# Kernel tuning notes

Hardware: AMD Instinct MI355X
Metric: run time of the kernel (lower is better)

## Reference

```python
import math
import numpy as np
import jax
import jax.numpy as jnp

B_IN, B_OUT, B_INV = 64, 20, 20
BATCH, F_IN, F_OUT = 16, 16, 32
N_GRID = 24
SCALING = 1.0 / math.sqrt(N_GRID * F_IN * B_OUT ** 4.0 / B_IN ** 2.0)


def _make_grid():
    # s2 near-identity grid: 3 betas (up to pi/8) x 8 alphas -> (beta, alpha) pairs
    beta = np.arange(1, 4) * (np.pi / 8) / 3
    alpha = np.linspace(0, 2 * np.pi, 8, endpoint=False)
    B, A = np.meshgrid(beta, alpha, indexing='ij')
    return np.stack((B.ravel(), A.ravel()), axis=1)  # [24, 2]


def _wigner_d(l, betas):
    """Full Wigner-d matrices d^l_{m,n}(beta): [n_beta, 2l+1, 2l+1], m,n in -l..l."""
    nb = betas.shape[0]
    cb, sb = np.cos(betas / 2.0), np.sin(betas / 2.0)
    lg = [math.lgamma(k + 1) for k in range(2 * l + 1)]
    d = np.zeros((nb, 2 * l + 1, 2 * l + 1))
    for mi, m in enumerate(range(-l, l + 1)):
        for ni, n in enumerate(range(-l, l + 1)):
            pref = 0.5 * (lg[l + m] + lg[l - m] + lg[l + n] + lg[l - n])
            val = np.zeros(nb)
            for s in range(max(0, n - m), min(l + n, l - m) + 1):
                c = pref - (lg[l + n - s] + lg[s] + lg[m - n + s] + lg[l - m - s])
                val += ((-1.0) ** (m - n + s)) * np.exp(c) * cb ** (2 * l + n - m - 2 * s) * sb ** (m - n + 2 * s)
            d[:, mi, ni] = val
    return d


def _quadrature_weights(b):
    # SOFT quadrature weights over the 2b beta samples
    k = np.arange(b)
    theta = np.pi * (2 * np.arange(2 * b) + 1) / (4.0 * b)
    return np.array([(2.0 / b) * np.sin(t) * np.sum(np.sin((2 * k + 1) * t) / (2 * k + 1)) for t in theta])


def _setup_constants():
    # S2 analysis weights: quadrature-weighted d^l_{m,0}(beta_j), laid out as l-blocks (start l^2, width 2l+1)
    betas_in = np.pi * (2 * np.arange(2 * B_IN) + 1) / (4.0 * B_IN)
    w = _quadrature_weights(B_IN)
    cols = [_wigner_d(l, betas_in)[:, :, l] * w[:, None] for l in range(B_OUT)]
    w_s2 = np.concatenate(cols, axis=1)  # [2*B_IN, B_OUT**2]

    # kernel spherical-harmonic sampling matrix F[p, lm] = d^l_{m,0}(beta_p) * exp(-i m alpha_p)
    grid = _make_grid()
    blocks = []
    for l in range(B_OUT):
        dk = _wigner_d(l, grid[:, 0])[:, :, l]  # [P, 2l+1]
        m = np.arange(-l, l + 1)
        blocks.append(dk * np.exp(-1j * m[None, :] * grid[:, 1:2]))
    F_k = np.concatenate(blocks, axis=1)  # [P, B_OUT**2] complex

    # SO(3) synthesis: (2l+1) * d^l_{m,n}(beta_j) on the output beta grid
    betas_inv = np.pi * (2 * np.arange(2 * B_INV) + 1) / (4.0 * B_INV)
    d_inv = [(2 * l + 1) * _wigner_d(l, betas_inv) for l in range(B_OUT)]
    return (jnp.asarray(w_s2, jnp.float32),
            jnp.asarray(F_k, jnp.complex64),
            [jnp.asarray(d, jnp.float32) for d in d_inv])


_CONSTS = None


def _consts():
    global _CONSTS
    if _CONSTS is None:
        _CONSTS = _setup_constants()
    return _CONSTS


def _forward(x, kernel, bias, w_s2, F_k, d_inv):
    # S2 FFT over alpha: x [batch, f_in, 2b_in(beta), 2b_in(alpha)] -> complex freq bins
    xf = jnp.fft.fft(x.astype(jnp.complex64), axis=-1)
    # kernel spectrum y^l_m: [nspec, f_in, f_out]
    y = jnp.einsum('iop,pm->mio', (kernel * SCALING).astype(jnp.complex64), F_k)
    two_b = 2 * B_INV
    out = jnp.zeros((x.shape[0], F_OUT, two_b, two_b, two_b), jnp.complex64)  # [z,o,beta,mfreq,nfreq]
    for l in range(B_OUT):
        sl = slice(l * l, (l + 1) * (l + 1))
        # gather alpha frequencies m = -l..l (negative freqs wrap to end of FFT bins)
        xx = jnp.concatenate((xf[..., -l:], xf[..., :l + 1]), axis=-1) if l > 0 else xf[..., :1]
        xl = jnp.einsum('bm,zibm->mzi', w_s2[:, sl], xx)        # S2 spectrum block [2l+1, batch, f_in]
        zl = jnp.einsum('mzi,nio->mnzo', xl, jnp.conj(y[sl]))   # SO3 spectrum block (s2_mm, conj on kernel)
        t = jnp.einsum('mnzo,bmn->zobmn', zl, d_inv[l])         # per-output-beta synthesis
        idx = jnp.arange(-l, l + 1) % two_b                     # place m,n into FFT bins
        out = out.at[:, :, :, idx[:, None], idx[None, :]].add(t)
    f = jnp.real(jnp.fft.ifft2(out, axes=(-2, -1))) * float(two_b ** 2)  # inverse over (alpha,gamma)
    return f + bias  # [batch, f_out, 2b_inv, 2b_inv, 2b_inv]


def setup_inputs() -> dict:
    key = jax.random.key(0)
    k1, k2 = jax.random.split(key)
    x = jax.random.normal(k1, (BATCH, F_IN, 2 * B_IN, 2 * B_IN), jnp.float32)
    kernel = jax.random.uniform(k2, (F_IN, F_OUT, N_GRID), jnp.float32, -1.0, 1.0)
    bias = jnp.zeros((1, F_OUT, 1, 1, 1), jnp.float32)
    return {"x": x, "kernel": kernel, "bias": bias}


def reference(x, kernel, bias):
    w_s2, F_k, d_inv = _consts()
    return _forward(x, kernel, bias, w_s2, F_k, d_inv)
```

## Files before the change

kernel.cpp:

```cpp
#include <hip/hip_runtime.h>
#include <math.h>

#define NB_IN   128
#define NBINS   39
#define NLM     400
#define NZO     512
#define NPAIR   780
#define NPACK   5530
#define TWOB    40
#define PI_D    3.14159265358979323846
#define SCALING 0.008164965809277261

__host__ __device__ __forceinline__ int lbase(int l){
  return l*(l-1)*(2*l-1)/3 + 3*l*(l-1)/2 + l;
}

__device__ __forceinline__ int lidx(int lm){
  int l = (int)sqrtf((float)lm);
  while ((l+1)*(l+1) <= lm) ++l;
  while (l*l > lm) --l;
  return l;
}

__device__ double wigner_d(int l, int m, int n, double beta, const double* lg){
  double cb = cos(0.5*beta), sb = sin(0.5*beta);
  double lcb = log(cb), lsb = log(sb);
  double pref = 0.5*(lg[l+m]+lg[l-m]+lg[l+n]+lg[l-n]);
  int s0 = 0 > (n-m) ? 0 : (n-m);
  int s1 = (l+n) < (l-m) ? (l+n) : (l-m);
  double val = 0.0;
  for (int s = s0; s <= s1; ++s){
    double c = pref - (lg[l+n-s]+lg[s]+lg[m-n+s]+lg[l-m-s]);
    double t = exp(c + (double)(2*l+n-m-2*s)*lcb + (double)(m-n+2*s)*lsb);
    val += ((m-n+s)&1) ? -t : t;
  }
  return val;
}

__device__ double wigner_fast(int l, int m, int n, double beta, const double* lg){
  double cb = cos(0.5*beta), sb = sin(0.5*beta);
  double lcb = log(cb), lsb = log(sb);
  double pref = 0.5*(lg[l+m]+lg[l-m]+lg[l+n]+lg[l-n]);
  int s0 = 0 > (n-m) ? 0 : (n-m);
  int s1 = (l+n) < (l-m) ? (l+n) : (l-m);
  double ratio = (sb*sb)/(cb*cb);
  double t = exp(pref - (lg[l+n-s0]+lg[s0]+lg[m-n+s0]+lg[l-m-s0])
               + (double)(2*l+n-m-2*s0)*lcb + (double)(m-n+2*s0)*lsb);
  double sgn = ((m-n+s0)&1) ? -1.0 : 1.0;
  double acc = 0.0;
  for (int s = s0; s <= s1; ++s){
    acc += sgn*t;
    sgn = -sgn;
    t *= ratio * ((double)((l+n-s)*(l-m-s)) / (double)((s+1)*(m-n+s+1)));
  }
  return acc;
}

__global__ void k_init(double* lg, double* wq, int* psort, int* ridx2, float2* wsyn){
  int t = threadIdx.x;
  if (t == 0){
    lg[0] = 0.0; double acc = 0.0;
    for (int k = 1; k <= 40; ++k){ acc += log((double)k); lg[k] = acc; }
  }
  for (int p = t; p < NPAIR; p += 256){
    int mj = p/39, njs = p%39, d = njs-19, ad = d<0?-d:d;
    int lam = mj > ad ? mj : ad;
    int pre = (lam==0) ? 0 : (2*lam-1)*lam;
    int rank = (mj < lam) ? (2*mj + ((njs==19+lam)?1:0))
                          : (2*lam + (njs-(19-lam)));
    int R = pre + rank;
    psort[R] = mj | (njs<<8);
    int info = mj | (njs<<8);
    for (int l = lam; l < 20; ++l)
      ridx2[lbase(l) + R] = info | (l<<16);
  }
  if (t < 128){
    double theta = PI_D*(2*t+1)/256.0;
    double s = 0.0;
    for (int k = 0; k < 64; ++k) s += sin((2*k+1)*theta)/(double)(2*k+1);
    wq[t] = (2.0/64.0)*sin(theta)*s;
  }
  for (int idx = t; idx < 1560; idx += 256){
    int njs = idx/40, g = idx%40;
    double ang = 2.0*PI_D*(double)(njs-19)*(double)g/40.0;
    wsyn[idx] = make_float2((float)cos(ang), (float)sin(ang));
  }
}

__global__ void k_tables(float* w_s2, float* dinv3, float2* Fc,
                         const int* ridx2, const double* lg, const double* wq){
  int bid = blockIdx.x, t = threadIdx.x;
  if (bid < 200){
    int tid = bid*256 + t;
    if (tid >= 128*NLM) return;
    int b = tid / NLM, lm = tid % NLM;
    int l = lidx(lm); int m = lm - l*l - l;
    double beta = PI_D*(2*b+1)/256.0;
    w_s2[b*NLM + lm] = (float)(wigner_fast(l, m, 0, beta, lg) * wq[b]);
  } else if (bid < 633){
    int idx = (bid-200)*256 + t;
    if (idx >= 20*NPACK) return;
    int b = idx / NPACK, k = idx % NPACK;
    int info = ridx2[k];
    int mj = info & 255, njs = (info>>8)&255, l = info>>16;
    int n = njs - 19, ad = n < 0 ? -n : n;
    int lam = mj > ad ? mj : ad;
    int pre = (lam==0) ? 0 : (2*lam-1)*lam;
    int rank_m = (mj < lam) ? (2*mj + ((njs == 19-lam) ? 1 : 0))
                            : (2*lam + (19 + lam - njs));
    float sgn = ((l+mj)&1) ? -1.f : 1.f;
    double beta = PI_D*(2*b+1)/80.0;
    float v = (float)((double)(2*l+1) * wigner_fast(l, mj, n, beta, lg));
    dinv3[b*NPACK + k] = v;
    dinv3[(39-b)*NPACK + lbase(l) + pre + rank_m] = sgn * v;
  } else {
    int tid = (bid-633)*256 + t;
    if (tid >= 24*NLM) return;
    int p = tid / NLM, lm = tid % NLM;
    int l = lidx(lm); int m = lm - l*l - l;
    double beta = PI_D*(double)(p/8 + 1)/24.0;
    double alpha = (double)(p%8)*(PI_D/4.0);
    double d = wigner_d(l, m, 0, beta, lg);
    double a = (double)m*alpha;
    Fc[tid] = make_float2((float)(d*cos(a)), (float)(d*sin(a)));
  }
}

__global__ void k_yc(const float* ker, const float2* Fc, float2* ycT){
  int tid = blockIdx.x*256 + threadIdx.x;
  if (tid >= NLM*NZO) return;
  int lm = tid / 512, io = tid % 512;
  int i = io >> 5, o = io & 31;
  float2 acc = make_float2(0.f, 0.f);
  for (int p = 0; p < 24; ++p){
    float kv = ker[io*24 + p];
    float2 f = Fc[p*NLM + lm];
    acc.x += kv*f.x; acc.y += kv*f.y;
  }
  acc.x *= (float)SCALING; acc.y *= (float)SCALING;
  ycT[((size_t)(o*16 + i))*NLM + lm] = acc;
}

__global__ __launch_bounds__(256) void k_dft(const float* x, float2* xf){
  __shared__ float rows[4][128];
  int t = threadIdx.x, g = t >> 6, lane = t & 63;
  int r = blockIdx.x*4 + g;
  int zi = r & 255, b = r >> 8;
  const float* xr = x + ((size_t)zi*128 + b)*128;
  rows[g][lane]    = xr[lane];
  rows[g][lane+64] = xr[lane+64];
  __syncthreads();
  if (lane < NBINS){
    int m = lane - 19;
    float th = -2.0f*(float)PI_D*(float)m/128.0f;
    float sn1, cs1; sincosf(th, &sn1, &cs1);
    float cs2 = cs1*cs1 - sn1*sn1, sn2 = 2.f*cs1*sn1;
    float cs4 = cs2*cs2 - sn2*sn2, sn4 = 2.f*cs2*sn2;
    float w0r = 1.f, w0i = 0.f;
    float w1r = cs1, w1i = sn1;
    float w2r = cs2, w2i = sn2;
    float w3r = cs1*cs2 - sn1*sn2, w3i = cs1*sn2 + sn1*cs2;
    float2 a0 = make_float2(0.f,0.f), a1 = a0, a2 = a0, a3 = a0;
    const float* rw = rows[g];
    #pragma unroll 4
    for (int q = 0; q < 32; ++q){
      float v0 = rw[4*q], v1 = rw[4*q+1], v2 = rw[4*q+2], v3 = rw[4*q+3];
      a0.x += v0*w0r; a0.y += v0*w0i;
      a1.x += v1*w1r; a1.y += v1*w1i;
      a2.x += v2*w2r; a2.y += v2*w2i;
      a3.x += v3*w3r; a3.y += v3*w3i;
      float nr;
      nr = w0r*cs4 - w0i*sn4; w0i = w0r*sn4 + w0i*cs4; w0r = nr;
      nr = w1r*cs4 - w1i*sn4; w1i = w1r*sn4 + w1i*cs4; w1r = nr;
      nr = w2r*cs4 - w2i*sn4; w2i = w2r*sn4 + w2i*cs4; w2r = nr;
      nr = w3r*cs4 - w3i*sn4; w3i = w3r*sn4 + w3i*cs4; w3r = nr;
    }
    float2 acc = make_float2(a0.x+a1.x+a2.x+a3.x, a0.y+a1.y+a2.y+a3.y);
    xf[((size_t)lane*128 + b)*256 + zi] = acc;
  }
}

__global__ void k_xlp(const float2* xf, const float* w_s2, float2* xlp){
  int lm = blockIdx.x, c = blockIdx.y, zi = threadIdx.x;
  int l = lidx(lm); int m = lm - l*l - l;
  int bin = m + 19;
  float2 acc = make_float2(0.f, 0.f);
  for (int b = c*32; b < c*32+32; ++b){
    float w = w_s2[b*NLM + lm];
    float2 v = xf[((size_t)bin*128 + b)*256 + zi];
    acc.x += w*v.x; acc.y += w*v.y;
  }
  xlp[((size_t)(c*NLM + lm))*256 + zi] = acc;
}

__global__ void k_xlsum(const float2* xlp, float2* xlT){
  int lm = blockIdx.x, zi = threadIdx.x;
  float2 s = make_float2(0.f, 0.f);
  for (int c = 0; c < 4; ++c){
    float2 v = xlp[((size_t)(c*NLM + lm))*256 + zi];
    s.x += v.x; s.y += v.y;
  }
  xlT[(size_t)zi*NLM + lm] = s;
}

__global__ void k_zl2s(const float2* xlT, const float2* ycT, const int* ridx2,
                       float2* z3){
  int tid = blockIdx.x*256 + threadIdx.x;
  if (tid >= NZO*NPACK) return;
  int zo = tid / NPACK, k = tid % NPACK;
  int info = ridx2[k];
  int mj = info & 255, njs = (info>>8)&255, l = info>>16;
  int z = zo >> 5, o = zo & 31;
  int lmm = l*l + l + mj;
  int lmn = l*l + l + (njs - 19);
  const float2* xrow = xlT + (size_t)(z*16)*NLM;
  const float2* yrow = ycT + (size_t)(o*16)*NLM;
  float2 acc = make_float2(0.f, 0.f);
  #pragma unroll 16
  for (int i = 0; i < 16; ++i){
    float2 a  = xrow[i*NLM + lmm];
    float2 bb = yrow[i*NLM + lmn];
    acc.x += a.x*bb.x - a.y*bb.y;
    acc.y += a.x*bb.y + a.y*bb.x;
  }
  z3[tid] = acc;
}

__global__ __launch_bounds__(256) void k_s1g(const float* dinv3, const float2* z3,
                                             const int* psort, float2* Cg){
  int tid = blockIdx.x*256 + threadIdx.x;
  if (tid >= NZO*NPAIR) return;
  int zo = tid / NPAIR, s = tid % NPAIR;
  int pk = psort[s];
  int mj = pk & 255, njs = (pk>>8)&255;
  int d_ = njs - 19, ad = d_ < 0 ? -d_ : d_;
  int lam = mj > ad ? mj : ad;
  const float2* zrow = z3 + (size_t)zo*NPACK;
  float2 zr[20];
  #pragma unroll
  for (int l = 0; l < 20; ++l){
    float2 v = zrow[lbase(l) + s];
    bool act = (l >= lam);
    zr[l].x = act ? v.x : 0.f;
    zr[l].y = act ? v.y : 0.f;
  }
  for (int b = 0; b < 40; ++b){
    const float* drow = dinv3 + (size_t)b*NPACK;
    float2 c = make_float2(0.f, 0.f);
    #pragma unroll
    for (int l = 0; l < 20; ++l){
      float dv = drow[lbase(l) + s];
      c.x += dv*zr[l].x;
      c.y += dv*zr[l].y;
    }
    Cg[((size_t)(zo*40 + b))*NPAIR + s] = c;
  }
}

__global__ __launch_bounds__(512) void k_s2(const float2* Cg, const int* psort,
                                            const float2* wsyn, const float* bias,
                                            float* out){
  __shared__ float2 Cs[2][NPAIR];
  __shared__ float2 Gs[2][800];
  __shared__ float2 Wq[390];
  __shared__ float2 Wma[200];
  int blk = blockIdx.x;
  int zo = blk / 20, bg = blk % 20;
  int b0 = bg*2;
  int o = zo & 31;
  int t = threadIdx.x;

  const float2* crow = Cg + (size_t)(zo*40 + b0)*NPAIR;
  for (int idx = t; idx < 2*NPAIR; idx += 512){
    int b_ = idx / NPAIR, p = idx % NPAIR;
    int pk = psort[p];
    Cs[b_][(pk&255)*39 + ((pk>>8)&255)] = crow[b_*NPAIR + p];
  }
  for (int idx = t; idx < 390; idx += 512){
    int njs = idx/10, g0 = idx%10;
    Wq[idx] = wsyn[njs*40 + g0];
  }
  for (int idx = t; idx < 200; idx += 512){
    int mj = idx/10, a0 = idx%10;
    Wma[idx] = wsyn[(19+mj)*40 + a0];
  }
  __syncthreads();

  if (t < 400){
    int b_ = t / 200, r2 = t % 200;
    int mj = r2 / 10, g0 = r2 % 10;
    const float2* cr = Cs[b_] + mj*39;
    float2 S0 = make_float2(0.f,0.f), S1 = S0, S2 = S0, S3 = S0;
    for (int j = 0; j < 9; ++j){
      float2 c = cr[3+4*j]; float2 w = Wq[(3+4*j)*10 + g0];
      S0.x += c.x*w.x - c.y*w.y; S0.y += c.x*w.y + c.y*w.x;
    }
    for (int j = 0; j < 10; ++j){
      float2 c = cr[4*j]; float2 w = Wq[(4*j)*10 + g0];
      S1.x += c.x*w.x - c.y*w.y; S1.y += c.x*w.y + c.y*w.x;
    }
    for (int j = 0; j < 10; ++j){
      float2 c = cr[1+4*j]; float2 w = Wq[(1+4*j)*10 + g0];
      S2.x += c.x*w.x - c.y*w.y; S2.y += c.x*w.y + c.y*w.x;
    }
    for (int j = 0; j < 10; ++j){
      float2 c = cr[2+4*j]; float2 w = Wq[(2+4*j)*10 + g0];
      S3.x += c.x*w.x - c.y*w.y; S3.y += c.x*w.y + c.y*w.x;
    }
    float2* gb = Gs[b_];
    gb[mj*40 + g0     ] = make_float2(S0.x+S1.x+S2.x+S3.x, S0.y+S1.y+S2.y+S3.y);
    gb[mj*40 + g0 + 10] = make_float2(S0.x-S1.y-S2.x+S3.y, S0.y+S1.x-S2.y-S3.x);
    gb[mj*40 + g0 + 20] = make_float2(S0.x-S1.x+S2.x-S3.x, S0.y-S1.y+S2.y-S3.y);
    gb[mj*40 + g0 + 30] = make_float2(S0.x+S1.y-S2.x-S3.y, S0.y-S1.x-S2.y+S3.x);
  }
  __syncthreads();

  float bv = bias[o];
  for (int idx = t; idx < 800; idx += 512){
    int b_ = idx / 400, r3 = idx % 400;
    int a0 = r3 / 40, g = r3 % 40;
    const float2* gb = Gs[b_];
    float S0x = 0.f, S2x = 0.f;
    float2 S1 = make_float2(0.f,0.f), S3 = S1;
    for (int j = 0; j < 4; ++j){
      float2 gv = gb[(4+4*j)*40 + g]; float2 w = Wma[(4+4*j)*10 + a0];
      S0x += gv.x*w.x - gv.y*w.y;
    }
    for (int j = 0; j < 5; ++j){
      float2 gv = gb[(1+4*j)*40 + g]; float2 w = Wma[(1+4*j)*10 + a0];
      S1.x += gv.x*w.x - gv.y*w.y; S1.y += gv.x*w.y + gv.y*w.x;
    }
    for (int j = 0; j < 5; ++j){
      float2 gv = gb[(2+4*j)*40 + g]; float2 w = Wma[(2+4*j)*10 + a0];
      S2x += gv.x*w.x - gv.y*w.y;
    }
    for (int j = 0; j < 5; ++j){
      float2 gv = gb[(3+4*j)*40 + g]; float2 w = Wma[(3+4*j)*10 + a0];
      S3.x += gv.x*w.x - gv.y*w.y; S3.y += gv.x*w.y + gv.y*w.x;
    }
    float g0v = gb[g].x;
    float* orow = out + ((size_t)zo*40 + b0 + b_)*1600;
    orow[(a0     )*40 + g] = g0v + 2.f*(S0x + S1.x + S2x + S3.x) + bv;
    orow[(a0 + 10)*40 + g] = g0v + 2.f*(S0x - S1.y - S2x + S3.y) + bv;
    orow[(a0 + 20)*40 + g] = g0v + 2.f*(S0x - S1.x + S2x - S3.x) + bv;
    orow[(a0 + 30)*40 + g] = g0v + 2.f*(S0x + S1.y - S2x - S3.y) + bv;
  }
}

extern "C" void kernel_launch(void* const* d_in, const int* in_sizes, int n_in,
                              void* d_out, int out_size, void* d_ws, size_t ws_size,
                              hipStream_t stream) {
  const float* x    = (const float*)d_in[0];
  const float* ker  = (const float*)d_in[1];
  const float* bias = (const float*)d_in[2];
  float* out = (float*)d_out;

  char* ws = (char*)d_ws;
  size_t cur = 0;
  auto alloc = [&](size_t bytes)->char*{
    char* p = ws + cur;
    cur += (bytes + 255) & ~(size_t)255;
    return p;
  };
  double* lg    = (double*)alloc(64*8);
  double* wq    = (double*)alloc(128*8);
  int*    psort = (int*)   alloc(NPAIR*4);
  int*    ridx2 = (int*)   alloc(NPACK*4);
  float2* wsyn  = (float2*)alloc((size_t)1560*8);
  float*  w_s2  = (float*) alloc((size_t)NB_IN*NLM*4);
  float*  dinv3 = (float*) alloc((size_t)TWOB*NPACK*4);
  float2* Fc    = (float2*)alloc((size_t)24*NLM*8);
  float2* ycT   = (float2*)alloc((size_t)512*400*8);
  float2* xf    = (float2*)alloc((size_t)NBINS*128*256*8);
  float2* xlp   = (float2*)alloc((size_t)4*NLM*256*8);
  float2* xlT   = (float2*)alloc((size_t)256*NLM*8);
  float2* z3    = (float2*)alloc((size_t)NZO*NPACK*8);
  float2* Cg    = (float2*)alloc((size_t)NZO*40*NPAIR*8);
  (void)ws_size; (void)in_sizes; (void)n_in; (void)out_size;

  k_init  <<<1, 256, 0, stream>>>(lg, wq, psort, ridx2, wsyn);
  k_tables<<<671, 256, 0, stream>>>(w_s2, dinv3, Fc, ridx2, lg, wq);
  k_yc    <<<800, 256, 0, stream>>>(ker, Fc, ycT);

  k_dft  <<<(256*128)/4, 256, 0, stream>>>(x, xf);
  k_xlp  <<<dim3(NLM, 4), 256, 0, stream>>>(xf, w_s2, xlp);
  k_xlsum<<<NLM, 256, 0, stream>>>(xlp, xlT);
  k_zl2s <<<(NZO*NPACK + 255)/256, 256, 0, stream>>>(xlT, ycT, ridx2, z3);
  k_s1g  <<<(NZO*NPAIR + 255)/256, 256, 0, stream>>>(dinv3, z3, psort, Cg);
  k_s2   <<<NZO*20, 512, 0, stream>>>(Cg, psort, wsyn, bias, out);
}
```

Baseline: 396.1 us.

## Split fused shared-memory synthesis kernel into two flat global-memory kernels

```diff
diff --git a/kernel.cpp b/kernel.cpp
--- a/kernel.cpp
+++ b/kernel.cpp
@@ -56,7 +56,8 @@
   return acc;
 }
 
-__global__ void k_init(double* lg, double* wq, int* psort, int* ridx2, float2* wsyn){
+__global__ void k_init(double* lg, double* wq, int* psort, int* ipsort,
+                       int* ridx2, float2* wsyn){
   int t = threadIdx.x;
   if (t == 0){
     lg[0] = 0.0; double acc = 0.0;
@@ -70,6 +71,7 @@
                           : (2*lam + (njs-(19-lam)));
     int R = pre + rank;
     psort[R] = mj | (njs<<8);
+    ipsort[p] = R;
     int info = mj | (njs<<8);
     for (int l = lam; l < 20; ++l)
       ridx2[lbase(l) + R] = info | (l<<16);
@@ -257,94 +259,79 @@
   }
 }
 
-__global__ __launch_bounds__(512) void k_s2(const float2* Cg, const int* psort,
-                                            const float2* wsyn, const float* bias,
-                                            float* out){
-  __shared__ float2 Cs[2][NPAIR];
-  __shared__ float2 Gs[2][800];
-  __shared__ float2 Wq[390];
-  __shared__ float2 Wma[200];
-  int blk = blockIdx.x;
-  int zo = blk / 20, bg = blk % 20;
-  int b0 = bg*2;
-  int o = zo & 31;
-  int t = threadIdx.x;
-
-  const float2* crow = Cg + (size_t)(zo*40 + b0)*NPAIR;
-  for (int idx = t; idx < 2*NPAIR; idx += 512){
-    int b_ = idx / NPAIR, p = idx % NPAIR;
-    int pk = psort[p];
-    Cs[b_][(pk&255)*39 + ((pk>>8)&255)] = crow[b_*NPAIR + p];
-  }
-  for (int idx = t; idx < 390; idx += 512){
-    int njs = idx/10, g0 = idx%10;
-    Wq[idx] = wsyn[njs*40 + g0];
-  }
-  for (int idx = t; idx < 200; idx += 512){
-    int mj = idx/10, a0 = idx%10;
-    Wma[idx] = wsyn[(19+mj)*40 + a0];
-  }
-  __syncthreads();
-
-  if (t < 400){
-    int b_ = t / 200, r2 = t % 200;
-    int mj = r2 / 10, g0 = r2 % 10;
-    const float2* cr = Cs[b_] + mj*39;
-    float2 S0 = make_float2(0.f,0.f), S1 = S0, S2 = S0, S3 = S0;
-    for (int j = 0; j < 9; ++j){
-      float2 c = cr[3+4*j]; float2 w = Wq[(3+4*j)*10 + g0];
-      S0.x += c.x*w.x - c.y*w.y; S0.y += c.x*w.y + c.y*w.x;
-    }
-    for (int j = 0; j < 10; ++j){
-      float2 c = cr[4*j]; float2 w = Wq[(4*j)*10 + g0];
-      S1.x += c.x*w.x - c.y*w.y; S1.y += c.x*w.y + c.y*w.x;
-    }
-    for (int j = 0; j < 10; ++j){
-      float2 c = cr[1+4*j]; float2 w = Wq[(1+4*j)*10 + g0];
-      S2.x += c.x*w.x - c.y*w.y; S2.y += c.x*w.y + c.y*w.x;
-    }
-    for (int j = 0; j < 10; ++j){
-      float2 c = cr[2+4*j]; float2 w = Wq[(2+4*j)*10 + g0];
-      S3.x += c.x*w.x - c.y*w.y; S3.y += c.x*w.y + c.y*w.x;
-    }
-    float2* gb = Gs[b_];
-    gb[mj*40 + g0     ] = make_float2(S0.x+S1.x+S2.x+S3.x, S0.y+S1.y+S2.y+S3.y);
-    gb[mj*40 + g0 + 10] = make_float2(S0.x-S1.y-S2.x+S3.y, S0.y+S1.x-S2.y-S3.x);
-    gb[mj*40 + g0 + 20] = make_float2(S0.x-S1.x+S2.x-S3.x, S0.y-S1.y+S2.y-S3.y);
-    gb[mj*40 + g0 + 30] = make_float2(S0.x+S1.y-S2.x-S3.y, S0.y-S1.x-S2.y+S3.x);
-  }
-  __syncthreads();
-
+__global__ __launch_bounds__(256) void k_g(const float2* Cg, const int* ipsort,
+                                           const float2* wsyn, float2* G){
+  int tid = blockIdx.x*256 + threadIdx.x;
+  if (tid >= NZO*40*200) return;
+  int item = tid % 200, zob = tid / 200;
+  int mj = item / 10, g0 = item % 10;
+  const float2* crow = Cg + (size_t)zob*NPAIR;
+  const int* ip = ipsort + mj*39;
+  float2 S0 = make_float2(0.f,0.f), S1 = S0, S2 = S0, S3 = S0;
+  for (int j = 0; j < 9; ++j){
+    int njs = 3+4*j;
+    float2 c = crow[ip[njs]]; float2 w = wsyn[njs*40 + g0];
+    S0.x += c.x*w.x - c.y*w.y; S0.y += c.x*w.y + c.y*w.x;
+  }
+  for (int j = 0; j < 10; ++j){
+    int njs = 4*j;
+    float2 c = crow[ip[njs]]; float2 w = wsyn[njs*40 + g0];
+    S1.x += c.x*w.x - c.y*w.y; S1.y += c.x*w.y + c.y*w.x;
+  }
+  for (int j = 0; j < 10; ++j){
+    int njs = 1+4*j;
+    float2 c = crow[ip[njs]]; float2 w = wsyn[njs*40 + g0];
+    S2.x += c.x*w.x - c.y*w.y; S2.y += c.x*w.y + c.y*w.x;
+  }
+  for (int j = 0; j < 10; ++j){
+    int njs = 2+4*j;
+    float2 c = crow[ip[njs]]; float2 w = wsyn[njs*40 + g0];
+    S3.x += c.x*w.x - c.y*w.y; S3.y += c.x*w.y + c.y*w.x;
+  }
+  float2* gb = G + (size_t)zob*800 + mj*40 + g0;
+  gb[ 0] = make_float2(S0.x+S1.x+S2.x+S3.x, S0.y+S1.y+S2.y+S3.y);
+  gb[10] = make_float2(S0.x-S1.y-S2.x+S3.y, S0.y+S1.x-S2.y-S3.x);
+  gb[20] = make_float2(S0.x-S1.x+S2.x-S3.x, S0.y-S1.y+S2.y-S3.y);
+  gb[30] = make_float2(S0.x+S1.y-S2.x-S3.y, S0.y-S1.x-S2.y+S3.x);
+}
+
+__global__ __launch_bounds__(256) void k_o(const float2* G, const float2* wsyn,
+                                           const float* bias, float* out){
+  int tid = blockIdx.x*256 + threadIdx.x;
+  if (tid >= NZO*40*400) return;
+  int item = tid % 400, zob = tid / 400;
+  int a0 = item / 40, g = item % 40;
+  int o = (zob / 40) & 31;
+  const float2* gb = G + (size_t)zob*800;
+  float S0x = 0.f, S2x = 0.f;
+  float2 S1 = make_float2(0.f,0.f), S3 = S1;
+  for (int j = 0; j < 4; ++j){
+    int mj = 4+4*j;
+    float2 gv = gb[mj*40 + g]; float2 w = wsyn[(19+mj)*40 + a0];
+    S0x += gv.x*w.x - gv.y*w.y;
+  }
+  for (int j = 0; j < 5; ++j){
+    int mj = 1+4*j;
+    float2 gv = gb[mj*40 + g]; float2 w = wsyn[(19+mj)*40 + a0];
+    S1.x += gv.x*w.x - gv.y*w.y; S1.y += gv.x*w.y + gv.y*w.x;
+  }
+  for (int j = 0; j < 5; ++j){
+    int mj = 2+4*j;
+    float2 gv = gb[mj*40 + g]; float2 w = wsyn[(19+mj)*40 + a0];
+    S2x += gv.x*w.x - gv.y*w.y;
+  }
+  for (int j = 0; j < 5; ++j){
+    int mj = 3+4*j;
+    float2 gv = gb[mj*40 + g]; float2 w = wsyn[(19+mj)*40 + a0];
+    S3.x += gv.x*w.x - gv.y*w.y; S3.y += gv.x*w.y + gv.y*w.x;
+  }
+  float g0v = gb[g].x;
   float bv = bias[o];
-  for (int idx = t; idx < 800; idx += 512){
-    int b_ = idx / 400, r3 = idx % 400;
-    int a0 = r3 / 40, g = r3 % 40;
-    const float2* gb = Gs[b_];
-    float S0x = 0.f, S2x = 0.f;
-    float2 S1 = make_float2(0.f,0.f), S3 = S1;
-    for (int j = 0; j < 4; ++j){
-      float2 gv = gb[(4+4*j)*40 + g]; float2 w = Wma[(4+4*j)*10 + a0];
-      S0x += gv.x*w.x - gv.y*w.y;
-    }
-    for (int j = 0; j < 5; ++j){
-      float2 gv = gb[(1+4*j)*40 + g]; float2 w = Wma[(1+4*j)*10 + a0];
-      S1.x += gv.x*w.x - gv.y*w.y; S1.y += gv.x*w.y + gv.y*w.x;
-    }
-    for (int j = 0; j < 5; ++j){
-      float2 gv = gb[(2+4*j)*40 + g]; float2 w = Wma[(2+4*j)*10 + a0];
-      S2x += gv.x*w.x - gv.y*w.y;
-    }
-    for (int j = 0; j < 5; ++j){
-      float2 gv = gb[(3+4*j)*40 + g]; float2 w = Wma[(3+4*j)*10 + a0];
-      S3.x += gv.x*w.x - gv.y*w.y; S3.y += gv.x*w.y + gv.y*w.x;
-    }
-    float g0v = gb[g].x;
-    float* orow = out + ((size_t)zo*40 + b0 + b_)*1600;
-    orow[(a0     )*40 + g] = g0v + 2.f*(S0x + S1.x + S2x + S3.x) + bv;
-    orow[(a0 + 10)*40 + g] = g0v + 2.f*(S0x - S1.y - S2x + S3.y) + bv;
-    orow[(a0 + 20)*40 + g] = g0v + 2.f*(S0x - S1.x + S2x - S3.x) + bv;
-    orow[(a0 + 30)*40 + g] = g0v + 2.f*(S0x + S1.y - S2x - S3.y) + bv;
-  }
+  float* orow = out + (size_t)zob*1600;
+  orow[(a0     )*40 + g] = g0v + 2.f*(S0x + S1.x + S2x + S3.x) + bv;
+  orow[(a0 + 10)*40 + g] = g0v + 2.f*(S0x - S1.y - S2x + S3.y) + bv;
+  orow[(a0 + 20)*40 + g] = g0v + 2.f*(S0x - S1.x + S2x - S3.x) + bv;
+  orow[(a0 + 30)*40 + g] = g0v + 2.f*(S0x + S1.y - S2x - S3.y) + bv;
 }
 
 extern "C" void kernel_launch(void* const* d_in, const int* in_sizes, int n_in,
@@ -362,23 +349,25 @@
     cur += (bytes + 255) & ~(size_t)255;
     return p;
   };
-  double* lg    = (double*)alloc(64*8);
-  double* wq    = (double*)alloc(128*8);
-  int*    psort = (int*)   alloc(NPAIR*4);
-  int*    ridx2 = (int*)   alloc(NPACK*4);
-  float2* wsyn  = (float2*)alloc((size_t)1560*8);
-  float*  w_s2  = (float*) alloc((size_t)NB_IN*NLM*4);
-  float*  dinv3 = (float*) alloc((size_t)TWOB*NPACK*4);
-  float2* Fc    = (float2*)alloc((size_t)24*NLM*8);
-  float2* ycT   = (float2*)alloc((size_t)512*400*8);
-  float2* xf    = (float2*)alloc((size_t)NBINS*128*256*8);
-  float2* xlp   = (float2*)alloc((size_t)4*NLM*256*8);
-  float2* xlT   = (float2*)alloc((size_t)256*NLM*8);
-  float2* z3    = (float2*)alloc((size_t)NZO*NPACK*8);
-  float2* Cg    = (float2*)alloc((size_t)NZO*40*NPAIR*8);
+  double* lg     = (double*)alloc(64*8);
+  double* wq     = (double*)alloc(128*8);
+  int*    psort  = (int*)   alloc(NPAIR*4);
+  int*    ipsort = (int*)   alloc(NPAIR*4);
+  int*    ridx2  = (int*)   alloc(NPACK*4);
+  float2* wsyn   = (float2*)alloc((size_t)1560*8);
+  float*  w_s2   = (float*) alloc((size_t)NB_IN*NLM*4);
+  float*  dinv3  = (float*) alloc((size_t)TWOB*NPACK*4);
+  float2* Fc     = (float2*)alloc((size_t)24*NLM*8);
+  float2* ycT    = (float2*)alloc((size_t)512*400*8);
+  float2* xf     = (float2*)alloc((size_t)NBINS*128*256*8);
+  float2* xlp    = (float2*)alloc((size_t)4*NLM*256*8);
+  float2* xlT    = (float2*)alloc((size_t)256*NLM*8);
+  float2* z3     = (float2*)alloc((size_t)NZO*NPACK*8);
+  float2* Cg     = (float2*)alloc((size_t)NZO*40*NPAIR*8);
+  float2* G      = (float2*)alloc((size_t)NZO*40*800*8);
   (void)ws_size; (void)in_sizes; (void)n_in; (void)out_size;
 
-  k_init  <<<1, 256, 0, stream>>>(lg, wq, psort, ridx2, wsyn);
+  k_init  <<<1, 256, 0, stream>>>(lg, wq, psort, ipsort, ridx2, wsyn);
   k_tables<<<671, 256, 0, stream>>>(w_s2, dinv3, Fc, ridx2, lg, wq);
   k_yc    <<<800, 256, 0, stream>>>(ker, Fc, ycT);
 
@@ -387,5 +376,6 @@
   k_xlsum<<<NLM, 256, 0, stream>>>(xlp, xlT);
   k_zl2s <<<(NZO*NPACK + 255)/256, 256, 0, stream>>>(xlT, ycT, ridx2, z3);
   k_s1g  <<<(NZO*NPAIR + 255)/256, 256, 0, stream>>>(dinv3, z3, psort, Cg);
-  k_s2   <<<NZO*20, 512, 0, stream>>>(Cg, psort, wsyn, bias, out);
-}
+  k_g    <<<(NZO*40*200 + 255)/256, 256, 0, stream>>>(Cg, ipsort, wsyn, G);
+  k_o    <<<(NZO*40*400 + 255)/256, 256, 0, stream>>>(G, wsyn, bias, out);
+}
```

Result: slower. 599.9 us (+51.5%).
